# Optimization experiments

Hardware: AMD Instinct MI355X
Metric: run time of the kernel (lower is better)

## Reference

```python
import jax, jax.numpy as jnp
import numpy as np

H = 16  # n_heads

def setup_inputs() -> dict:
    key = jax.random.key(0)
    k1, k2, k3, k4 = jax.random.split(key, 4)
    B, S, D = 2, 2048, 1024
    query = jax.random.normal(k1, (B, S, D), dtype=jnp.float32)
    pos_emb = jax.random.normal(k2, (S, D), dtype=jnp.float32)
    w_qkv = jax.random.normal(k3, (D, 3 * D), dtype=jnp.float32) * (D ** -0.5)
    w_out = jax.random.normal(k4, (D, D), dtype=jnp.float32) * (D ** -0.5)
    return {"query": query, "pos_emb": pos_emb, "w_qkv": w_qkv, "w_out": w_out}

def reference(query, pos_emb, w_qkv, w_out):
    B, S, D = query.shape
    d_k = D // H
    # ape=True: pos_fn applied to input before QKV projection (additive APE)
    x = query + pos_emb[None, :, :]
    # fused QKV projection; torch view(B,S,H,3*d_k) + chunk(3,-1) == reshape(B,S,H,3,d_k)
    qkv = jnp.einsum('bsd,de->bse', x, w_qkv).reshape(B, S, H, 3, d_k)
    qkv = jnp.transpose(qkv, (0, 2, 1, 3, 4))  # [B,H,S,3,d_k]
    q, k, v = qkv[..., 0, :], qkv[..., 1, :], qkv[..., 2, :]
    scale = d_k ** -0.5
    scores = jnp.einsum('bhqd,bhkd->bhqk', q, k) * scale  # [B,H,S,S]
    attn = jax.nn.softmax(scores, axis=-1)  # dropout is identity in eval
    o = jnp.einsum('bhqk,bhkd->bhqd', attn, v)
    o = jnp.transpose(o, (0, 2, 1, 3)).reshape(B, S, D)
    return jnp.einsum('bsd,de->bse', o, w_out)
```

## Files before the change

kernel.cpp:

```cpp
#include <hip/hip_runtime.h>

#define SS 2048
#define DD 1024
#define N3 3072

typedef unsigned short u16;
typedef unsigned int u32;
typedef __attribute__((ext_vector_type(8))) short bf16x8;
typedef __attribute__((ext_vector_type(4))) float f32x4;

__device__ __forceinline__ u16 f2bf(float f) {
    u32 u = __float_as_uint(f);
    u32 r = u + 0x7fffu + ((u >> 16) & 1u);
    return (u16)(r >> 16);
}

__device__ __forceinline__ u32 pack2bf(float x, float y) {
    return (u32)f2bf(x) | ((u32)f2bf(y) << 16);
}

__device__ __forceinline__ float fast_exp2(float x) {
    return __builtin_amdgcn_exp2f(x);
}

__device__ __forceinline__ void async_cp16(u16* lds, const u16* g) {
    __builtin_amdgcn_global_load_lds((const __attribute__((address_space(1))) u32*)g,
                                     (__attribute__((address_space(3))) u32*)lds, 16, 0, 0);
}

__global__ __launch_bounds__(256)
void prep_x(const float* __restrict__ q, const float* __restrict__ pos, u16* __restrict__ x)
{
    const size_t i = ((size_t)blockIdx.x * 256 + threadIdx.x) * 4;
    float4 a = *(const float4*)(q + i);
    float4 p = *(const float4*)(pos + (i & (size_t)(SS * DD - 1)));
    uint2 r;
    r.x = pack2bf(a.x + p.x, a.y + p.y);
    r.y = pack2bf(a.z + p.z, a.w + p.w);
    *(uint2*)(x + i) = r;
}

__global__ __launch_bounds__(256)
void transpose_bf16(const float* __restrict__ W, u16* __restrict__ WT, int K, int N)
{
    __shared__ float t[32][33];
    const int tx = threadIdx.x & 31, ty = threadIdx.x >> 5;
    const int x0 = blockIdx.x * 32, y0 = blockIdx.y * 32;
#pragma unroll
    for (int i = 0; i < 4; ++i)
        t[ty + i * 8][tx] = W[(size_t)(y0 + ty + i * 8) * N + x0 + tx];
    __syncthreads();
#pragma unroll
    for (int i = 0; i < 4; ++i)
        WT[(size_t)(x0 + ty + i * 8) * K + y0 + tx] = f2bf(t[tx][ty + i * 8]);
}

template <int OUT_BF16, int NT>
__global__ __launch_bounds__(256)
void gemm_mfma(const u16* __restrict__ A, const u16* __restrict__ BT,
               void* __restrict__ Cv, int M, int N, int K)
{
    constexpr int FR = NT / 32;
    __shared__ u16 As[128 * 64];
    __shared__ u16 Bs[NT * 64];

    const int tid = threadIdx.x;
    const int lane = tid & 63, wv = tid >> 6;
    const int quad = lane >> 4, l16 = lane & 15;
    const int m0 = blockIdx.y * 128, n0 = blockIdx.x * NT;

    const int arow = wv * 32 + (lane >> 3);
    const int pc   = lane & 7;
    const int lcA  = pc ^ (arow & 7);
    const u16* agp = A + (size_t)(m0 + arow) * K + lcA * 8;
    u16* alp = As + arow * 64 + pc * 8;

    const int brow = (NT == 128) ? (wv * 32 + (lane >> 3)) : (wv * 8 + (lane >> 3));
    const int lcB  = pc ^ (brow & 7);
    const u16* bgp = BT + (size_t)(n0 + brow) * K + lcB * 8;
    u16* blp = Bs + brow * 64 + pc * 8;

    const int moff = (wv >> 1) * 64, noff = (wv & 1) * (NT / 2);

    f32x4 acc[4][FR];
#pragma unroll
    for (int i = 0; i < 4; ++i)
#pragma unroll
        for (int j = 0; j < FR; ++j) acc[i][j] = {0.f, 0.f, 0.f, 0.f};

    const int swf = l16 & 7;

    for (int k0 = 0; k0 < K; k0 += 64) {
#pragma unroll
        for (int s = 0; s < 4; ++s)
            async_cp16(alp + s * 8 * 64, agp + (size_t)(s * 8) * K + k0);
        if constexpr (NT == 128) {
#pragma unroll
            for (int s = 0; s < 4; ++s)
                async_cp16(blp + s * 8 * 64, bgp + (size_t)(s * 8) * K + k0);
        } else {
#pragma unroll
            for (int s = 0; s < 2; ++s)
                async_cp16(blp + s * 32 * 64, bgp + (size_t)(s * 32) * K + k0);
        }
        __syncthreads();

#pragma unroll
        for (int ks = 0; ks < 2; ++ks) {
            bf16x8 af[4], bfr[FR];
#pragma unroll
            for (int t = 0; t < 4; ++t)
                af[t] = *(const bf16x8*)&As[(moff + t * 16 + l16) * 64 + (((ks * 4 + quad) ^ swf) << 3)];
#pragma unroll
            for (int t = 0; t < FR; ++t)
                bfr[t] = *(const bf16x8*)&Bs[(noff + t * 16 + l16) * 64 + (((ks * 4 + quad) ^ swf) << 3)];
#pragma unroll
            for (int mt = 0; mt < 4; ++mt)
#pragma unroll
                for (int nt = 0; nt < FR; ++nt)
                    acc[mt][nt] = __builtin_amdgcn_mfma_f32_16x16x32_bf16(af[mt], bfr[nt], acc[mt][nt], 0, 0, 0);
        }
        __syncthreads();
    }

#pragma unroll
    for (int mt = 0; mt < 4; ++mt)
#pragma unroll
        for (int r = 0; r < 4; ++r) {
            const size_t row = m0 + moff + mt * 16 + quad * 4 + r;
            if (OUT_BF16) {
                u16* cp = (u16*)Cv + row * N + n0 + noff + l16;
#pragma unroll
                for (int nt = 0; nt < FR; ++nt) cp[nt * 16] = f2bf(acc[mt][nt][r]);
            } else {
                float* cp = (float*)Cv + row * N + n0 + noff + l16;
#pragma unroll
                for (int nt = 0; nt < FR; ++nt) cp[nt * 16] = acc[mt][nt][r];
            }
        }
}

__global__ __launch_bounds__(256)
void attn_mfma(const u16* __restrict__ qkv, u16* __restrict__ o)
{
    __shared__ u16 Ks[64 * 64];
    __shared__ u16 Vn[64 * 64];
    __shared__ u16 Vt[64 * 64];
    __shared__ u16 Ps[4][32 * 64];

    const int tid = threadIdx.x;
    const int lane = tid & 63, wv = tid >> 6;
    const int quad = lane >> 4, l16 = lane & 15;
    const int bx = blockIdx.x;
    const int h = bx & 15, b = (bx >> 4) & 1, qt = bx >> 5;

    const size_t hb = (size_t)b * SS * N3 + h * 192;
    const int q0 = qt * 128 + wv * 32;
    const int sw = l16 & 7;

    bf16x8 qf[2][2];
#pragma unroll
    for (int mt = 0; mt < 2; ++mt)
#pragma unroll
        for (int ks = 0; ks < 2; ++ks)
            qf[mt][ks] = *(const bf16x8*)(qkv + hb + (size_t)(q0 + mt * 16 + l16) * N3 + ks * 32 + quad * 8);

    f32x4 po[2][4];
#pragma unroll
    for (int mt = 0; mt < 2; ++mt)
#pragma unroll
        for (int nt = 0; nt < 4; ++nt) po[mt][nt] = {0.f, 0.f, 0.f, 0.f};
    float lrun[2] = {0.f, 0.f};

    const int skey = tid >> 2;
    const int sc16 = (tid & 3) * 16;
    const int c0 = (tid & 3) * 2;
    const u16* kg = qkv + hb + 64 + (size_t)skey * N3 + sc16;
    const u16* vg = kg + 64;
    const int ksw = skey & 7;
    u16* kst0 = &Ks[skey * 64 + (((c0    ) ^ ksw) << 3)];
    u16* kst1 = &Ks[skey * 64 + (((c0 + 1) ^ ksw) << 3)];
    u16* vst0 = &Vn[skey * 64 + (((c0    ) ^ ksw) << 3)];
    u16* vst1 = &Vn[skey * 64 + (((c0 + 1) ^ ksw) << 3)];

    const int kp = tid & 31, dkb = (tid >> 5) * 8;

    const float CEXP = 0.125f * 1.44269504f;

    uint4 kv0 = *(const uint4*)kg;
    uint4 kv1 = *(const uint4*)(kg + 8);
    uint4 vv0 = *(const uint4*)vg;
    uint4 vv1 = *(const uint4*)(vg + 8);

    for (int kt = 0; kt < SS / 64; ++kt) {
        *(uint4*)kst0 = kv0;  *(uint4*)kst1 = kv1;
        *(uint4*)vst0 = vv0;  *(uint4*)vst1 = vv1;
        __syncthreads();

        if (kt + 1 < SS / 64) {
            const size_t koff = (size_t)(kt + 1) * 64 * N3;
            kv0 = *(const uint4*)(kg + koff);
            kv1 = *(const uint4*)(kg + koff + 8);
            vv0 = *(const uint4*)(vg + koff);
            vv1 = *(const uint4*)(vg + koff + 8);
        }

        {
            uint4 a4 = *(const uint4*)&Vn[(2 * kp)     * 64 + (((dkb >> 3) ^ ((2 * kp)     & 7)) << 3)];
            uint4 b4 = *(const uint4*)&Vn[(2 * kp + 1) * 64 + (((dkb >> 3) ^ ((2 * kp + 1) & 7)) << 3)];
            u32 ar[4] = {a4.x, a4.y, a4.z, a4.w};
            u32 br[4] = {b4.x, b4.y, b4.z, b4.w};
#pragma unroll
            for (int j = 0; j < 8; ++j) {
                const u32 sel = (j & 1) ? 0x07060302u : 0x05040100u;
                const u32 w = __builtin_amdgcn_perm(br[j >> 1], ar[j >> 1], sel);
                const int row = dkb + j;
                *(u32*)&Vt[row * 64 + (((kp >> 2) ^ (row & 7)) << 3) + ((2 * kp) & 7)] = w;
            }
        }

        f32x4 sf[2][4];
#pragma unroll
        for (int mt = 0; mt < 2; ++mt)
#pragma unroll
            for (int kn = 0; kn < 4; ++kn) sf[mt][kn] = {0.f, 0.f, 0.f, 0.f};
#pragma unroll
        for (int ks = 0; ks < 2; ++ks)
#pragma unroll
            for (int kn = 0; kn < 4; ++kn) {
                bf16x8 kf = *(const bf16x8*)&Ks[(kn * 16 + l16) * 64 + (((ks * 4 + quad) ^ sw) << 3)];
#pragma unroll
                for (int mt = 0; mt < 2; ++mt)
                    sf[mt][kn] = __builtin_amdgcn_mfma_f32_16x16x32_bf16(kf, qf[mt][ks], sf[mt][kn], 0, 0, 0);
            }

#pragma unroll
        for (int mt = 0; mt < 2; ++mt) {
            float ls = 0.f;
#pragma unroll
            for (int kn = 0; kn < 4; ++kn) {
                const float p0 = fast_exp2(sf[mt][kn][0] * CEXP);
                const float p1 = fast_exp2(sf[mt][kn][1] * CEXP);
                const float p2 = fast_exp2(sf[mt][kn][2] * CEXP);
                const float p3 = fast_exp2(sf[mt][kn][3] * CEXP);
                const u32 w0 = __builtin_amdgcn_perm(__float_as_uint(p1), __float_as_uint(p0), 0x07060302u);
                const u32 w1 = __builtin_amdgcn_perm(__float_as_uint(p3), __float_as_uint(p2), 0x07060302u);
                ls += __uint_as_float(w0 << 16) + __uint_as_float(w0 & 0xffff0000u)
                    + __uint_as_float(w1 << 16) + __uint_as_float(w1 & 0xffff0000u);
                const int ch = (2 * kn + (quad >> 1)) ^ sw;
                uint2 wp; wp.x = w0; wp.y = w1;
                *(uint2*)&Ps[wv][(mt * 16 + l16) * 64 + (ch << 3) + ((quad & 1) << 2)] = wp;
            }
            lrun[mt] += ls;
        }
        __syncthreads();

#pragma unroll
        for (int ks = 0; ks < 2; ++ks) {
            bf16x8 pf[2], vf[4];
#pragma unroll
            for (int mt = 0; mt < 2; ++mt)
                pf[mt] = *(const bf16x8*)&Ps[wv][(mt * 16 + l16) * 64 + (((ks * 4 + quad) ^ sw) << 3)];
#pragma unroll
            for (int nt = 0; nt < 4; ++nt)
                vf[nt] = *(const bf16x8*)&Vt[(nt * 16 + l16) * 64 + (((ks * 4 + quad) ^ sw) << 3)];
#pragma unroll
            for (int mt = 0; mt < 2; ++mt)
#pragma unroll
                for (int nt = 0; nt < 4; ++nt)
                    po[mt][nt] = __builtin_amdgcn_mfma_f32_16x16x32_bf16(pf[mt], vf[nt], po[mt][nt], 0, 0, 0);
        }
        __syncthreads();
    }

#pragma unroll
    for (int mt = 0; mt < 2; ++mt) {
        lrun[mt] += __shfl_xor(lrun[mt], 16, 64);
        lrun[mt] += __shfl_xor(lrun[mt], 32, 64);
    }
#pragma unroll
    for (int mt = 0; mt < 2; ++mt) {
        float linv[4];
#pragma unroll
        for (int r = 0; r < 4; ++r)
            linv[r] = 1.f / __shfl(lrun[mt], quad * 4 + r, 64);
#pragma unroll
        for (int r = 0; r < 4; ++r) {
            const size_t row = (size_t)b * SS + q0 + mt * 16 + quad * 4 + r;
            u16* op = o + row * DD + h * 64 + l16;
#pragma unroll
            for (int nt = 0; nt < 4; ++nt)
                op[nt * 16] = f2bf(po[mt][nt][r] * linv[r]);
        }
    }
}

extern "C" void kernel_launch(void* const* d_in, const int* in_sizes, int n_in,
                              void* d_out, int out_size, void* d_ws, size_t ws_size,
                              hipStream_t stream)
{
    const float* query  = (const float*)d_in[0];
    const float* posemb = (const float*)d_in[1];
    const float* w_qkv  = (const float*)d_in[2];
    const float* w_out  = (const float*)d_in[3];
    float* out = (float*)d_out;

    u16* xb    = (u16*)d_ws;
    u16* wqkvT = xb    + (size_t)4096 * 1024;
    u16* woutT = wqkvT + (size_t)3072 * 1024;
    u16* qkv   = woutT + (size_t)1024 * 1024;
    u16* ob    = qkv   + (size_t)4096 * 3072;

    prep_x<<<4096, 256, 0, stream>>>(query, posemb, xb);
    transpose_bf16<<<dim3(N3 / 32, DD / 32), 256, 0, stream>>>(w_qkv, wqkvT, DD, N3);
    transpose_bf16<<<dim3(DD / 32, DD / 32), 256, 0, stream>>>(w_out, woutT, DD, DD);

    gemm_mfma<1, 128><<<dim3(N3 / 128, 4096 / 128), 256, 0, stream>>>(xb, wqkvT, (void*)qkv, 4096, N3, DD);

    attn_mfma<<<dim3(512, 1, 1), 256, 0, stream>>>(qkv, ob);

    gemm_mfma<0, 64><<<dim3(DD / 64, 4096 / 128), 256, 0, stream>>>(ob, woutT, (void*)out, 4096, DD, DD);
}
```

Baseline: 205.2 us.

## Merge prep kernels into one launch and register-prefetch GEMM tiles

Folds the activation add/convert kernel and both weight-transpose kernels into a single launch that dispatches on block index, removing two kernel launches. The GEMM drops the direct global-to-LDS async copies. It now prefetches the next K tile into registers while computing the current one, then stores those registers to LDS at the start of the next iteration. This uses more registers and adds a register-to-LDS store step, in exchange for overlapping global loads with MFMA work.

```diff
diff --git a/kernel.cpp b/kernel.cpp
--- a/kernel.cpp
+++ b/kernel.cpp
@@ -23,29 +23,30 @@
     return __builtin_amdgcn_exp2f(x);
 }
 
-__device__ __forceinline__ void async_cp16(u16* lds, const u16* g) {
-    __builtin_amdgcn_global_load_lds((const __attribute__((address_space(1))) u32*)g,
-                                     (__attribute__((address_space(3))) u32*)lds, 16, 0, 0);
-}
-
 __global__ __launch_bounds__(256)
-void prep_x(const float* __restrict__ q, const float* __restrict__ pos, u16* __restrict__ x)
-{
-    const size_t i = ((size_t)blockIdx.x * 256 + threadIdx.x) * 4;
-    float4 a = *(const float4*)(q + i);
-    float4 p = *(const float4*)(pos + (i & (size_t)(SS * DD - 1)));
-    uint2 r;
-    r.x = pack2bf(a.x + p.x, a.y + p.y);
-    r.y = pack2bf(a.z + p.z, a.w + p.w);
-    *(uint2*)(x + i) = r;
-}
-
-__global__ __launch_bounds__(256)
-void transpose_bf16(const float* __restrict__ W, u16* __restrict__ WT, int K, int N)
+void prep_all(const float* __restrict__ q, const float* __restrict__ pos,
+              u16* __restrict__ x,
+              const float* __restrict__ w_qkv, u16* __restrict__ wqkvT,
+              const float* __restrict__ w_out, u16* __restrict__ woutT)
 {
     __shared__ float t[32][33];
+    const int bx = blockIdx.x;
+    if (bx < 4096) {
+        const size_t i = ((size_t)bx * 256 + threadIdx.x) * 4;
+        float4 a = *(const float4*)(q + i);
+        float4 p = *(const float4*)(pos + (i & (size_t)(SS * DD - 1)));
+        uint2 r;
+        r.x = pack2bf(a.x + p.x, a.y + p.y);
+        r.y = pack2bf(a.z + p.z, a.w + p.w);
+        *(uint2*)(x + i) = r;
+        return;
+    }
+    const float* W;  u16* WT;  int K, N, bid;
+    if (bx < 4096 + 3072) { bid = bx - 4096; W = w_qkv; WT = wqkvT; K = DD; N = N3; }
+    else                  { bid = bx - 7168; W = w_out; WT = woutT; K = DD; N = DD; }
+    const int bxx = bid % (N / 32), byy = bid / (N / 32);
     const int tx = threadIdx.x & 31, ty = threadIdx.x >> 5;
-    const int x0 = blockIdx.x * 32, y0 = blockIdx.y * 32;
+    const int x0 = bxx * 32, y0 = byy * 32;
 #pragma unroll
     for (int i = 0; i < 4; ++i)
         t[ty + i * 8][tx] = W[(size_t)(y0 + ty + i * 8) * N + x0 + tx];
@@ -61,6 +62,8 @@
                void* __restrict__ Cv, int M, int N, int K)
 {
     constexpr int FR = NT / 32;
+    constexpr int NB = (NT == 128) ? 4 : 2;
+    constexpr int BSTRIDE = (NT == 128) ? 8 : 32;
     __shared__ u16 As[128 * 64];
     __shared__ u16 Bs[NT * 64];
 
@@ -90,20 +93,31 @@
 
     const int swf = l16 & 7;
 
+    uint4 apf[4], bpf[NB];
+#pragma unroll
+    for (int s = 0; s < 4; ++s)
+        apf[s] = *(const uint4*)(agp + (size_t)(s * 8) * K);
+#pragma unroll
+    for (int s = 0; s < NB; ++s)
+        bpf[s] = *(const uint4*)(bgp + (size_t)(s * BSTRIDE) * K);
+
     for (int k0 = 0; k0 < K; k0 += 64) {
 #pragma unroll
         for (int s = 0; s < 4; ++s)
-            async_cp16(alp + s * 8 * 64, agp + (size_t)(s * 8) * K + k0);
-        if constexpr (NT == 128) {
+            *(uint4*)(alp + s * 8 * 64) = apf[s];
+#pragma unroll
+        for (int s = 0; s < NB; ++s)
+            *(uint4*)(blp + s * BSTRIDE * 64) = bpf[s];
+        __syncthreads();
+
+        if (k0 + 64 < K) {
 #pragma unroll
             for (int s = 0; s < 4; ++s)
-                async_cp16(blp + s * 8 * 64, bgp + (size_t)(s * 8) * K + k0);
-        } else {
-#pragma unroll
-            for (int s = 0; s < 2; ++s)
-                async_cp16(blp + s * 32 * 64, bgp + (size_t)(s * 32) * K + k0);
-        }
-        __syncthreads();
+                apf[s] = *(const uint4*)(agp + (size_t)(s * 8) * K + k0 + 64);
+#pragma unroll
+            for (int s = 0; s < NB; ++s)
+                bpf[s] = *(const uint4*)(bgp + (size_t)(s * BSTRIDE) * K + k0 + 64);
+        }
 
 #pragma unroll
         for (int ks = 0; ks < 2; ++ks) {
@@ -311,9 +325,7 @@
     u16* qkv   = woutT + (size_t)1024 * 1024;
     u16* ob    = qkv   + (size_t)4096 * 3072;
 
-    prep_x<<<4096, 256, 0, stream>>>(query, posemb, xb);
-    transpose_bf16<<<dim3(N3 / 32, DD / 32), 256, 0, stream>>>(w_qkv, wqkvT, DD, N3);
-    transpose_bf16<<<dim3(DD / 32, DD / 32), 256, 0, stream>>>(w_out, woutT, DD, DD);
+    prep_all<<<8192, 256, 0, stream>>>(query, posemb, xb, w_qkv, wqkvT, w_out, woutT);
 
     gemm_mfma<1, 128><<<dim3(N3 / 128, 4096 / 128), 256, 0, stream>>>(xb, wqkvT, (void*)qkv, 4096, N3, DD);
 
```

After: 314.4 us. +53.2%, slower.
